# Kernel optimization log

Hardware: AMD Instinct MI355X
Metric: run time of the kernel (lower is better)

## Reference

```python
import jax, jax.numpy as jnp
from jax import lax
import numpy as np

B, T, C = 16, 2048, 1024
H, K = 16, 31
R = C // H
P = K - 1  # padding_l (causal)


def setup_inputs() -> dict:
    key = jax.random.key(0)
    kx, kw = jax.random.split(key)
    x = jax.random.normal(kx, (B, T, C), dtype=jnp.float32)
    # kaiming_uniform_(a=sqrt(5)) on (H, 1, K): fan_in = K, bound = 1/sqrt(K)
    bound = 1.0 / np.sqrt(K)
    weight = jax.random.uniform(kw, (H, 1, K), dtype=jnp.float32,
                                minval=-bound, maxval=bound)
    return {"x": x, "weight": weight}


def reference(x, weight):
    # weight_softmax=True: softmax over kernel dim (done in fp32, as in source)
    w = jax.nn.softmax(weight.reshape(H, K).astype(jnp.float32), axis=-1)
    w = w.astype(x.dtype)
    # Each head's kernel is shared across R = C//H channels -> depthwise kernel (C, 1, K)
    w_c = jnp.repeat(w, R, axis=0)            # (C, K)
    kernel = w_c[:, None, :]                  # (C, 1, K) in OIH layout
    x_t = jnp.transpose(x, (0, 2, 1))         # (B, C, T)
    # Cross-correlation with left pad P, right pad K-1-P (same math as the
    # banded-matrix _forward_expanded path / unfold1d + matmul)
    out = lax.conv_general_dilated(
        x_t, kernel,
        window_strides=(1,),
        padding=[(P, K - 1 - P)],
        feature_group_count=C,
        dimension_numbers=("NCH", "OIH", "NCH"),
    )                                         # (B, C, T)
    return jnp.transpose(out, (0, 2, 1))      # (B, T, C)
```

## Files before the change

kernel.cpp:

```cpp
#include <hip/hip_runtime.h>
#include <math.h>

#define TPB   64
#define KW    31
#define HALO  30
#define TT    8
#define WROWS 32
#define SROWS 64
constexpr int B_ = 16, T_ = 2048, C_ = 1024, H_ = 16;
constexpr int C4 = C_ / 4;

typedef float f32x4 __attribute__((ext_vector_type(4)));

__device__ inline float rfl(float v) {
    return __builtin_bit_cast(float, __builtin_amdgcn_readfirstlane(__builtin_bit_cast(int, v)));
}

__global__ __launch_bounds__(TPB) void lconv_kernel(const float* __restrict__ x,
                                                    const float* __restrict__ w,
                                                    float* __restrict__ out) {
    __shared__ float smem[SROWS * 64];
    const int h    = blockIdx.x;
    const int y    = blockIdx.y;
    const int b    = blockIdx.z;
    const int t0   = y * WROWS;
    const int lane = threadIdx.x;
    const int qrow = lane >> 4, chunk = lane & 15;
    const int quad = lane & 15, sl = lane >> 2 >> 2;

    const float* xh = x + (size_t)b * T_ * C_ + h * 64;
    #pragma unroll
    for (int q = 0; q < 16; ++q) {
        const int tq = t0 - 32 + 4 * q;
        if (tq >= 0) {
            const float* src = xh + (size_t)(tq + qrow) * C_ + chunk * 4;
            __builtin_amdgcn_global_load_lds(
                (const __attribute__((address_space(1))) uint32_t*)src,
                (__attribute__((address_space(3))) uint32_t*)(smem + q * 256),
                16, 0, 0);
        }
    }

    float wv[KW];
    {
        float v[KW]; float m = -1e30f;
        #pragma unroll
        for (int k = 0; k < KW; ++k) { v[k] = w[h * KW + k]; m = fmaxf(m, v[k]); }
        float s = 0.f;
        #pragma unroll
        for (int k = 0; k < KW; ++k) { v[k] = __expf(v[k] - m); s += v[k]; }
        const float inv = 1.f / s;
        #pragma unroll
        for (int j = 0; j < KW; ++j) wv[j] = rfl(v[KW - 1 - j] * inv);
    }

    if (y == 0) {
        f32x4* s4 = (f32x4*)smem;
        #pragma unroll
        for (int k = 0; k < 8; ++k) s4[k * 64 + lane] = (f32x4)0.f;
    }

    asm volatile("s_waitcnt vmcnt(0) lgkmcnt(0)" ::: "memory");
    __builtin_amdgcn_sched_barrier(0);

    f32x4 acc[TT];
    #pragma unroll
    for (int i = 0; i < TT; ++i) acc[i] = (f32x4)0.f;

    const f32x4* sm4 = (const f32x4*)smem;
    #pragma unroll
    for (int sr = 0; sr < TT + HALO; ++sr) {
        const f32x4 v = sm4[(8 * sl + 2 + sr) * 16 + quad];
        const int ilo = (sr - HALO < 0) ? 0 : sr - HALO;
        const int ihi = (sr < TT - 1) ? sr : TT - 1;
        #pragma unroll
        for (int i = ilo; i <= ihi; ++i) {
            acc[i] += wv[i + HALO - sr] * v;
        }
    }

    f32x4* po = (f32x4*)out + ((size_t)b * T_ + t0 + 8 * sl) * C4 + h * 16 + quad;
    #pragma unroll
    for (int i = 0; i < TT; ++i)
        __builtin_nontemporal_store(acc[i], po + (size_t)i * C4);
}

extern "C" void kernel_launch(void* const* d_in, const int* in_sizes, int n_in,
                              void* d_out, int out_size, void* d_ws, size_t ws_size,
                              hipStream_t stream) {
    const float* x = (const float*)d_in[0];
    const float* w = (const float*)d_in[1];
    float* out = (float*)d_out;

    dim3 grid(H_, T_ / WROWS, B_);
    hipLaunchKernelGGL(lconv_kernel, grid, dim3(TPB), 0, stream, x, w, out);
}
```

Before: 46.65 us.

## Stream each block over a long time segment with triple-buffered LDS halo reuse

Each workgroup now walks a 512-step time segment in 32-row chunks instead of handling one 32-row tile. A three-slot LDS ring prefetches the next chunk asynchronously while the current one is computed, and the halo rows are reused from the previous chunk rather than reloaded. This is meant to remove the roughly 2x read amplification of per-tile halo loads and to overlap global loads with compute. In exchange the grid shrinks to 1024 single-wave blocks, which lowers occupancy and the parallelism available to hide latency. Correctness relies on hand-counted vmcnt waits that also count the stores.

```diff
diff --git a/kernel.cpp b/kernel.cpp
--- a/kernel.cpp
+++ b/kernel.cpp
@@ -5,8 +5,9 @@
 #define KW    31
 #define HALO  30
 #define TT    8
-#define WROWS 32
-#define SROWS 64
+#define CH    32
+#define SEG   512
+#define NTILE (SEG / CH)
 constexpr int B_ = 16, T_ = 2048, C_ = 1024, H_ = 16;
 constexpr int C4 = C_ / 4;
 
@@ -19,27 +20,31 @@
 __global__ __launch_bounds__(TPB) void lconv_kernel(const float* __restrict__ x,
                                                     const float* __restrict__ w,
                                                     float* __restrict__ out) {
-    __shared__ float smem[SROWS * 64];
+    __shared__ float smem[3 * CH * 64];
     const int h    = blockIdx.x;
-    const int y    = blockIdx.y;
+    const int seg  = blockIdx.y;
     const int b    = blockIdx.z;
-    const int t0   = y * WROWS;
+    const int ts   = seg * SEG;
     const int lane = threadIdx.x;
     const int qrow = lane >> 4, chunk = lane & 15;
-    const int quad = lane & 15, sl = lane >> 2 >> 2;
+    const int quad = lane & 15, sl = lane >> 4;
 
     const float* xh = x + (size_t)b * T_ * C_ + h * 64;
-    #pragma unroll
-    for (int q = 0; q < 16; ++q) {
-        const int tq = t0 - 32 + 4 * q;
-        if (tq >= 0) {
-            const float* src = xh + (size_t)(tq + qrow) * C_ + chunk * 4;
+
+    auto stageChunk = [&](const int slot, const int row0) {
+        float* dst = smem + slot * (CH * 64);
+        #pragma unroll
+        for (int q = 0; q < 8; ++q) {
+            const float* src = xh + (size_t)(row0 + 4 * q + qrow) * C_ + chunk * 4;
             __builtin_amdgcn_global_load_lds(
                 (const __attribute__((address_space(1))) uint32_t*)src,
-                (__attribute__((address_space(3))) uint32_t*)(smem + q * 256),
+                (__attribute__((address_space(3))) uint32_t*)(dst + q * 256),
                 16, 0, 0);
         }
-    }
+    };
+
+    if (ts > 0) stageChunk(2, ts - CH);
+    stageChunk(0, ts);
 
     float wv[KW];
     {
@@ -54,35 +59,54 @@
         for (int j = 0; j < KW; ++j) wv[j] = rfl(v[KW - 1 - j] * inv);
     }
 
-    if (y == 0) {
-        f32x4* s4 = (f32x4*)smem;
+    if (ts == 0) {
+        f32x4* s4 = (f32x4*)(smem + 2 * (CH * 64));
         #pragma unroll
         for (int k = 0; k < 8; ++k) s4[k * 64 + lane] = (f32x4)0.f;
     }
 
-    asm volatile("s_waitcnt vmcnt(0) lgkmcnt(0)" ::: "memory");
-    __builtin_amdgcn_sched_barrier(0);
+    int slotA = 2, slotB = 0, slotN = 1;
 
-    f32x4 acc[TT];
-    #pragma unroll
-    for (int i = 0; i < TT; ++i) acc[i] = (f32x4)0.f;
+    #pragma unroll 1
+    for (int j = 0; j < NTILE; ++j) {
+        if (j + 1 < NTILE) stageChunk(slotN, ts + CH * (j + 1));
+        __builtin_amdgcn_sched_barrier(0);
 
-    const f32x4* sm4 = (const f32x4*)smem;
-    #pragma unroll
-    for (int sr = 0; sr < TT + HALO; ++sr) {
-        const f32x4 v = sm4[(8 * sl + 2 + sr) * 16 + quad];
-        const int ilo = (sr - HALO < 0) ? 0 : sr - HALO;
-        const int ihi = (sr < TT - 1) ? sr : TT - 1;
+        if (j == 0)
+            asm volatile("s_waitcnt vmcnt(8) lgkmcnt(0)" ::: "memory");
+        else if (j == NTILE - 1)
+            asm volatile("s_waitcnt vmcnt(8)" ::: "memory");
+        else
+            asm volatile("s_waitcnt vmcnt(16)" ::: "memory");
+        __builtin_amdgcn_sched_barrier(0);
+
+        const f32x4* pa = (const f32x4*)(smem + slotA * (CH * 64));
+        const f32x4* pb = (const f32x4*)(smem + slotB * (CH * 64));
+
+        f32x4 acc[TT];
         #pragma unroll
-        for (int i = ilo; i <= ihi; ++i) {
-            acc[i] += wv[i + HALO - sr] * v;
+        for (int i = 0; i < TT; ++i) acc[i] = (f32x4)0.f;
+
+        #pragma unroll
+        for (int sr = 0; sr < TT + HALO; ++sr) {
+            const int r = 8 * sl + 2 + sr;
+            const f32x4 v = (r < CH) ? pa[r * 16 + quad] : pb[(r - CH) * 16 + quad];
+            const int ilo = (sr - HALO < 0) ? 0 : sr - HALO;
+            const int ihi = (sr < TT - 1) ? sr : TT - 1;
+            #pragma unroll
+            for (int i = ilo; i <= ihi; ++i) {
+                acc[i] += wv[i + HALO - sr] * v;
+            }
         }
+
+        const int t0 = ts + CH * j;
+        f32x4* po = (f32x4*)out + ((size_t)b * T_ + t0 + 8 * sl) * C4 + h * 16 + quad;
+        #pragma unroll
+        for (int i = 0; i < TT; ++i)
+            __builtin_nontemporal_store(acc[i], po + (size_t)i * C4);
+
+        const int tmp = slotA; slotA = slotB; slotB = slotN; slotN = tmp;
     }
-
-    f32x4* po = (f32x4*)out + ((size_t)b * T_ + t0 + 8 * sl) * C4 + h * 16 + quad;
-    #pragma unroll
-    for (int i = 0; i < TT; ++i)
-        __builtin_nontemporal_store(acc[i], po + (size_t)i * C4);
 }
 
 extern "C" void kernel_launch(void* const* d_in, const int* in_sizes, int n_in,
@@ -92,6 +116,6 @@
     const float* w = (const float*)d_in[1];
     float* out = (float*)d_out;
 
-    dim3 grid(H_, T_ / WROWS, B_);
+    dim3 grid(H_, T_ / SEG, B_);
     hipLaunchKernelGGL(lconv_kernel, grid, dim3(TPB), 0, stream, x, w, out);
 }
```

Measured after the change: 50.54 us. +8.4%, slower.
